# Kernel optimization log

Measured on AMD Instinct MI355X. Metric: run time of the kernel, lower is better.

## Reference

```python
import jax, jax.numpy as jnp
import numpy as np

B, S, D = 4, 2048, 1024


def setup_inputs() -> dict:
    key = jax.random.key(0)
    k1, k2, k3, k4 = jax.random.split(key, 4)
    scale = 1.0 / np.sqrt(D)
    return {
        "X_emb": jax.random.normal(k1, (B, S, D), dtype=jnp.float32),
        "W_q": jax.random.normal(k2, (D, D), dtype=jnp.float32) * scale,
        "W_k": jax.random.normal(k3, (D, D), dtype=jnp.float32) * scale,
        "W_v": jax.random.normal(k4, (D, D), dtype=jnp.float32) * scale,
    }


def reference(X_emb, W_q, W_k, W_v):
    # nn.Linear(bias=False): x @ W.T
    Xq = jnp.einsum('bsd,ed->bse', X_emb, W_q)
    Xk = jnp.einsum('bsd,ed->bse', X_emb, W_k)
    Xv = jnp.einsum('bsd,ed->bse', X_emb, W_v)
    S_len = X_emb.shape[-2]
    # scores [B, S, S]; causal mask (strict upper triangle -> -inf)
    att = jnp.einsum('bqe,bke->bqk', Xq, Xk)
    causal = jnp.tril(jnp.ones((S_len, S_len), dtype=bool))
    att = jnp.where(causal, att, -jnp.inf)
    # note: original masks before scaling; -inf / sqrt(d) is still -inf
    att = att / jnp.sqrt(jnp.asarray(Xk.shape[-1], att.dtype))
    w = jax.nn.softmax(att, axis=-1)
    return jnp.einsum('bqk,bke->bqe', w, Xv)
```

## Files before the change

kernel.cpp:

```cpp
#include <hip/hip_runtime.h>
#include <stdint.h>
#include <math.h>

typedef __attribute__((ext_vector_type(8))) __bf16 bf16x8;
typedef __attribute__((ext_vector_type(4))) float f32x4;

__device__ __forceinline__ unsigned short f2bf(float f) {
    unsigned u = __float_as_uint(f);
    u += 0x7FFF + ((u >> 16) & 1);
    return (unsigned short)(u >> 16);
}

__global__ __launch_bounds__(256)
void f32_to_bf16_k(const float* __restrict__ in, unsigned short* __restrict__ out, int n4) {
    int i = blockIdx.x * blockDim.x + threadIdx.x;
    int stride = gridDim.x * blockDim.x;
    for (; i < n4; i += stride) {
        float4 v = reinterpret_cast<const float4*>(in)[i];
        ushort4 o;
        o.x = f2bf(v.x); o.y = f2bf(v.y); o.z = f2bf(v.z); o.w = f2bf(v.w);
        reinterpret_cast<ushort4*>(out)[i] = o;
    }
}

__global__ __launch_bounds__(256)
void w_convert_k(const float* __restrict__ Wq, const float* __restrict__ Wk,
                 const float* __restrict__ Wv, unsigned short* __restrict__ out, int n4) {
    const float* src = blockIdx.y == 0 ? Wq : (blockIdx.y == 1 ? Wk : Wv);
    unsigned short* dst = out + (size_t)blockIdx.y * n4 * 4;
    int i = blockIdx.x * blockDim.x + threadIdx.x;
    int stride = gridDim.x * blockDim.x;
    for (; i < n4; i += stride) {
        float4 v = reinterpret_cast<const float4*>(src)[i];
        ushort4 o;
        o.x = f2bf(v.x); o.y = f2bf(v.y); o.z = f2bf(v.z); o.w = f2bf(v.w);
        reinterpret_cast<ushort4*>(dst)[i] = o;
    }
}

__device__ __forceinline__ void gload16(const unsigned short* g, unsigned short* l) {
    __builtin_amdgcn_global_load_lds(
        (const __attribute__((address_space(1))) unsigned int*)g,
        (__attribute__((address_space(3))) unsigned int*)l, 16, 0, 0);
}

template <typename CT, int MODE>
__global__ __launch_bounds__(256, 2)
void gemm8(const unsigned short* __restrict__ A, const unsigned short* __restrict__ B,
           CT* __restrict__ C, int lda, int ldb, int ldc, int K,
           long long sA, long long sB, long long sC, float scale, int totj)
{
    constexpr int BM = 128, BN = 128;
    constexpr int FM = 4, FN = 4;

    const int nbx = gridDim.x;
    const int nwg = nbx * gridDim.y;
    const int orig = blockIdx.y * nbx + blockIdx.x;
    const int q8 = nwg >> 3, r8 = nwg & 7;
    const int xcd = orig & 7, idx = orig >> 3;
    const int work = (xcd < r8 ? xcd * (q8 + 1) : r8 * (q8 + 1) + (xcd - r8) * q8) + idx;

    A += (long long)blockIdx.z * sA;
    B += (long long)blockIdx.z * sB;
    C += (long long)blockIdx.z * sC;

    __shared__ unsigned short As[2][BM * 64];
    __shared__ unsigned short Bs[2][BN * 64];

    const int t    = threadIdx.x;
    const int lane = t & 63;
    const int wid  = t >> 6;
    const int wm   = wid >> 1, wn = wid & 1;
    const int rsel = lane & 15;
    const int gsel = lane >> 4;
    const int srow = t >> 3;
    const int swz  = ((t & 7) ^ (srow & 7)) * 8;

    auto run_tile = [&](int br, int bc, int kmax, bool first) {
        const int m0 = br * BM, n0 = bc * BN;
        f32x4 acc[FM][FN];
#pragma unroll
        for (int m = 0; m < FM; ++m)
#pragma unroll
            for (int n = 0; n < FN; ++n) acc[m][n] = (f32x4){0.f, 0.f, 0.f, 0.f};

        const unsigned short* gpA[4];
        const unsigned short* gpB[4];
#pragma unroll
        for (int i = 0; i < 4; ++i) {
            gpA[i] = A + (long long)(m0 + srow + 32 * i) * lda + swz;
            gpB[i] = B + (long long)(n0 + srow + 32 * i) * ldb + swz;
        }

        auto stage = [&](int buf) {
#pragma unroll
            for (int i = 0; i < 4; ++i)
                gload16(gpA[i], &As[buf][i * 2048 + t * 8]);
#pragma unroll
            for (int i = 0; i < 4; ++i)
                gload16(gpB[i], &Bs[buf][i * 2048 + t * 8]);
#pragma unroll
            for (int i = 0; i < 4; ++i) { gpA[i] += 64; gpB[i] += 64; }
        };

        const int nk = kmax >> 6;
        if (!first) {
            __builtin_amdgcn_s_barrier();
            __builtin_amdgcn_sched_barrier(0);
        }
        stage(0);

        for (int kt = 0; kt < nk; ++kt) {
            const int c = kt & 1;
            __builtin_amdgcn_s_barrier();
            __builtin_amdgcn_sched_barrier(0);
            if (kt + 1 < nk) {
                stage(c ^ 1);
                asm volatile("s_waitcnt vmcnt(8)" ::: "memory");
            } else {
                asm volatile("s_waitcnt vmcnt(0)" ::: "memory");
            }
            __builtin_amdgcn_s_barrier();
            __builtin_amdgcn_sched_barrier(0);

            bf16x8 aF[FM][2], bF[FN][2];
#pragma unroll
            for (int m = 0; m < FM; ++m)
#pragma unroll
                for (int ks = 0; ks < 2; ++ks) {
                    int r  = wm * (FM * 16) + m * 16 + rsel;
                    int cc = ks * 4 + gsel;
                    aF[m][ks] = *reinterpret_cast<const bf16x8*>(
                        &As[c][r * 64 + ((cc ^ (r & 7)) * 8)]);
                }
#pragma unroll
            for (int n = 0; n < FN; ++n)
#pragma unroll
                for (int ks = 0; ks < 2; ++ks) {
                    int rb = wn * (FN * 16) + n * 16 + rsel;
                    int cc = ks * 4 + gsel;
                    bF[n][ks] = *reinterpret_cast<const bf16x8*>(
                        &Bs[c][rb * 64 + ((cc ^ (rb & 7)) * 8)]);
                }

            __builtin_amdgcn_s_setprio(1);
#pragma unroll
            for (int m = 0; m < FM; ++m)
#pragma unroll
                for (int n = 0; n < FN; ++n)
#pragma unroll
                    for (int ks = 0; ks < 2; ++ks)
                        acc[m][n] = __builtin_amdgcn_mfma_f32_16x16x32_bf16(
                            aF[m][ks], bF[n][ks], acc[m][n], 0, 0, 0);
            __builtin_amdgcn_s_setprio(0);
        }

        const int rowl = gsel * 4;
#pragma unroll
        for (int m = 0; m < FM; ++m) {
#pragma unroll
            for (int n = 0; n < FN; ++n) {
#pragma unroll
                for (int i = 0; i < 4; ++i) {
                    int r  = m0 + wm * (FM * 16) + m * 16 + rowl + i;
                    int cI = n0 + wn * (FN * 16) + n * 16 + rsel;
                    float v = acc[m][n][i] * scale;
                    if constexpr (sizeof(CT) == 2)
                        ((unsigned short*)C)[(long long)r * ldc + cI] = f2bf(v);
                    else
                        ((float*)C)[(long long)r * ldc + cI] = v;
                }
            }
        }
    };

    auto tri = [&](int w, int& br, int& bc) {
        int rr = (int)((sqrtf(8.0f * (float)w + 1.0f) - 1.0f) * 0.5f);
        while ((rr + 1) * (rr + 2) / 2 <= w) ++rr;
        while (rr * (rr + 1) / 2 > w) --rr;
        br = rr; bc = w - rr * (rr + 1) / 2;
    };

    if constexpr (MODE == 0) {
        run_tile(work / nbx, work % nbx, K, true);
    } else if constexpr (MODE == 1) {
        int br, bc;
        tri(work, br, bc);
        run_tile(br, bc, K, true);
        const int e = work >> 4;
        if ((work & 15) == 8 && nwg + e < totj) {
            tri(nwg + e, br, bc);
            run_tile(br, bc, K, false);
        }
    } else {
        const int s = work & 1, pp = work >> 1;
        const int col = pp & 7, rp = pp >> 3;
        const int row = s ? 15 - rp : rp;
        run_tile(row, col, (row + 1) * BM, true);
    }
}

__device__ __forceinline__ float waveMax(float v) {
#pragma unroll
    for (int o = 32; o > 0; o >>= 1) v = fmaxf(v, __shfl_xor(v, o, 64));
    return v;
}
__device__ __forceinline__ float waveSum(float v) {
#pragma unroll
    for (int o = 32; o > 0; o >>= 1) v += __shfl_xor(v, o, 64);
    return v;
}

__global__ __launch_bounds__(256)
void softmax_causal(const float* __restrict__ S, unsigned short* __restrict__ P, int Slen) {
    __shared__ float e[2048];
    __shared__ float red[4];
    long long row = blockIdx.x;
    int q = (int)(row % Slen);
    const float* srow = S + row * (long long)Slen;
    unsigned short* prow = P + row * (long long)Slen;
    int len = q + 1;
    int t = threadIdx.x;

    int nfull = len >> 2;
    float mx = -3.0e38f;
    for (int i = t; i < nfull; i += 256) {
        float4 v = reinterpret_cast<const float4*>(srow)[i];
        e[4 * i + 0] = v.x; e[4 * i + 1] = v.y;
        e[4 * i + 2] = v.z; e[4 * i + 3] = v.w;
        mx = fmaxf(fmaxf(fmaxf(mx, v.x), v.y), fmaxf(v.z, v.w));
    }
    if (t < (len & 3)) {
        float v = srow[nfull * 4 + t];
        e[nfull * 4 + t] = v;
        mx = fmaxf(mx, v);
    }
    mx = waveMax(mx);
    if ((t & 63) == 0) red[t >> 6] = mx;
    __syncthreads();
    mx = fmaxf(fmaxf(red[0], red[1]), fmaxf(red[2], red[3]));

    float sum = 0.f;
    for (int k = t; k < len; k += 256) {
        float v = __expf(e[k] - mx);
        e[k] = v;
        sum += v;
    }
    sum = waveSum(sum);
    __syncthreads();
    if ((t & 63) == 0) red[t >> 6] = sum;
    __syncthreads();
    sum = red[0] + red[1] + red[2] + red[3];
    float inv = 1.0f / sum;

    int wlim = ((q >> 7) + 1) << 7;
    __syncthreads();
    for (int i = t; i < (wlim >> 2); i += 256) {
        int k = 4 * i;
        ushort4 o;
        o.x = (k + 0 < len) ? f2bf(e[k + 0] * inv) : (unsigned short)0;
        o.y = (k + 1 < len) ? f2bf(e[k + 1] * inv) : (unsigned short)0;
        o.z = (k + 2 < len) ? f2bf(e[k + 2] * inv) : (unsigned short)0;
        o.w = (k + 3 < len) ? f2bf(e[k + 3] * inv) : (unsigned short)0;
        reinterpret_cast<ushort4*>(prow)[i] = o;
    }
}

extern "C" void kernel_launch(void* const* d_in, const int* in_sizes, int n_in,
                              void* d_out, int out_size, void* d_ws, size_t ws_size,
                              hipStream_t stream) {
    const int B = 4, S = 2048, D = 1024;
    const float* X  = (const float*)d_in[0];
    const float* Wq = (const float*)d_in[1];
    const float* Wk = (const float*)d_in[2];
    const float* Wv = (const float*)d_in[3];
    float* out = (float*)d_out;

    char* ws = (char*)d_ws;
    unsigned short* Xb  = (unsigned short*)ws; ws += (size_t)B * S * D * 2;
    unsigned short* Wqb = (unsigned short*)ws; ws += (size_t)D * D * 2;
    unsigned short* Wkb = (unsigned short*)ws; ws += (size_t)D * D * 2;
    unsigned short* Wvb = (unsigned short*)ws; ws += (size_t)D * D * 2;
    unsigned short* Qb  = (unsigned short*)ws; ws += (size_t)B * S * D * 2;
    unsigned short* Kb  = (unsigned short*)ws; ws += (size_t)B * S * D * 2;
    unsigned short* Vt  = (unsigned short*)ws; ws += (size_t)B * S * D * 2;
    float*          Sc  = (float*)ws;          ws += (size_t)B * S * S * 4;
    unsigned short* P   = (unsigned short*)ws; ws += (size_t)B * S * S * 2;

    f32_to_bf16_k<<<2048, 256, 0, stream>>>(X, Xb, B * S * D / 4);
    w_convert_k<<<dim3(512, 3), 256, 0, stream>>>(Wq, Wk, Wv, Wqb, D * D / 4);

    dim3 blk(256);
    gemm8<unsigned short, 0><<<dim3(D / 128, B * S / 128, 2), blk, 0, stream>>>(
        Xb, Wqb, Qb, D, D, D, D, 0, (long long)D * D, (long long)B * S * D, 1.0f, 0);

    gemm8<unsigned short, 0><<<dim3(S / 128, D / 128, B), blk, 0, stream>>>(
        Wvb, Xb, Vt, D, D, S, D, 0, (long long)S * D, (long long)D * S, 1.0f, 0);

    gemm8<float, 1><<<dim3(8, 16, B), blk, 0, stream>>>(
        Qb, Kb, Sc, D, D, S, D, (long long)S * D, (long long)S * D, (long long)S * S,
        0.03125f, 136);

    softmax_causal<<<B * S, 256, 0, stream>>>(Sc, P, S);

    gemm8<float, 3><<<dim3(8, 16, B), blk, 0, stream>>>(
        P, Vt, out, S, S, D, S, (long long)S * S, (long long)D * S, (long long)S * D,
        1.0f, 0);
}
```

Baseline: 176.1 us.

## Deepen GEMM pipeline to four K=32 stages and store scores in bf16

Measured after the change: 203.6 us. +15.6%, slower.

```diff
diff --git a/kernel.cpp b/kernel.cpp
--- a/kernel.cpp
+++ b/kernel.cpp
@@ -9,6 +9,9 @@
     unsigned u = __float_as_uint(f);
     u += 0x7FFF + ((u >> 16) & 1);
     return (unsigned short)(u >> 16);
+}
+__device__ __forceinline__ float bf2f(unsigned short u) {
+    return __uint_as_float((unsigned)u << 16);
 }
 
 __global__ __launch_bounds__(256)
@@ -64,8 +67,8 @@
     B += (long long)blockIdx.z * sB;
     C += (long long)blockIdx.z * sC;
 
-    __shared__ unsigned short As[2][BM * 64];
-    __shared__ unsigned short Bs[2][BN * 64];
+    __shared__ unsigned short As[4][BM * 32];
+    __shared__ unsigned short Bs[4][BN * 32];
 
     const int t    = threadIdx.x;
     const int lane = t & 63;
@@ -73,8 +76,8 @@
     const int wm   = wid >> 1, wn = wid & 1;
     const int rsel = lane & 15;
     const int gsel = lane >> 4;
-    const int srow = t >> 3;
-    const int swz  = ((t & 7) ^ (srow & 7)) * 8;
+    const int srow = t >> 2;
+    const int swz  = ((t & 3) ^ (srow & 3)) * 8;
 
     auto run_tile = [&](int br, int bc, int kmax, bool first) {
         const int m0 = br * BM, n0 = bc * BN;
@@ -84,74 +87,64 @@
 #pragma unroll
             for (int n = 0; n < FN; ++n) acc[m][n] = (f32x4){0.f, 0.f, 0.f, 0.f};
 
-        const unsigned short* gpA[4];
-        const unsigned short* gpB[4];
-#pragma unroll
-        for (int i = 0; i < 4; ++i) {
-            gpA[i] = A + (long long)(m0 + srow + 32 * i) * lda + swz;
-            gpB[i] = B + (long long)(n0 + srow + 32 * i) * ldb + swz;
-        }
-
+        const unsigned short* gpA[2];
+        const unsigned short* gpB[2];
+#pragma unroll
+        for (int i = 0; i < 2; ++i) {
+            gpA[i] = A + (long long)(m0 + srow + 64 * i) * lda + swz;
+            gpB[i] = B + (long long)(n0 + srow + 64 * i) * ldb + swz;
+        }
         auto stage = [&](int buf) {
-#pragma unroll
-            for (int i = 0; i < 4; ++i)
-                gload16(gpA[i], &As[buf][i * 2048 + t * 8]);
-#pragma unroll
-            for (int i = 0; i < 4; ++i)
-                gload16(gpB[i], &Bs[buf][i * 2048 + t * 8]);
-#pragma unroll
-            for (int i = 0; i < 4; ++i) { gpA[i] += 64; gpB[i] += 64; }
+            gload16(gpA[0], &As[buf][t * 8]);
+            gload16(gpA[1], &As[buf][2048 + t * 8]);
+            gload16(gpB[0], &Bs[buf][t * 8]);
+            gload16(gpB[1], &Bs[buf][2048 + t * 8]);
+            gpA[0] += 32; gpA[1] += 32; gpB[0] += 32; gpB[1] += 32;
         };
 
-        const int nk = kmax >> 6;
+        const int nk = kmax >> 5;
         if (!first) {
             __builtin_amdgcn_s_barrier();
             __builtin_amdgcn_sched_barrier(0);
         }
         stage(0);
+        if (1 < nk) stage(1);
+        if (2 < nk) stage(2);
 
         for (int kt = 0; kt < nk; ++kt) {
-            const int c = kt & 1;
+            const int c = kt & 3;
             __builtin_amdgcn_s_barrier();
             __builtin_amdgcn_sched_barrier(0);
-            if (kt + 1 < nk) {
-                stage(c ^ 1);
-                asm volatile("s_waitcnt vmcnt(8)" ::: "memory");
-            } else {
-                asm volatile("s_waitcnt vmcnt(0)" ::: "memory");
-            }
+            if (kt + 3 < nk) stage((kt + 3) & 3);
+            const int rem = nk - 1 - kt;
+            if (rem >= 3)      asm volatile("s_waitcnt vmcnt(12)" ::: "memory");
+            else if (rem == 2) asm volatile("s_waitcnt vmcnt(8)"  ::: "memory");
+            else if (rem == 1) asm volatile("s_waitcnt vmcnt(4)"  ::: "memory");
+            else               asm volatile("s_waitcnt vmcnt(0)"  ::: "memory");
             __builtin_amdgcn_s_barrier();
             __builtin_amdgcn_sched_barrier(0);
 
-            bf16x8 aF[FM][2], bF[FN][2];
+            bf16x8 aF[FM], bF[FN];
+#pragma unroll
+            for (int m = 0; m < FM; ++m) {
+                int r = wm * (FM * 16) + m * 16 + rsel;
+                aF[m] = *reinterpret_cast<const bf16x8*>(
+                    &As[c][r * 32 + ((gsel ^ (r & 3)) * 8)]);
+            }
+#pragma unroll
+            for (int n = 0; n < FN; ++n) {
+                int rb = wn * (FN * 16) + n * 16 + rsel;
+                bF[n] = *reinterpret_cast<const bf16x8*>(
+                    &Bs[c][rb * 32 + ((gsel ^ (rb & 3)) * 8)]);
+            }
+
+            __builtin_amdgcn_s_setprio(1);
 #pragma unroll
             for (int m = 0; m < FM; ++m)
 #pragma unroll
-                for (int ks = 0; ks < 2; ++ks) {
-                    int r  = wm * (FM * 16) + m * 16 + rsel;
-                    int cc = ks * 4 + gsel;
-                    aF[m][ks] = *reinterpret_cast<const bf16x8*>(
-                        &As[c][r * 64 + ((cc ^ (r & 7)) * 8)]);
-                }
-#pragma unroll
-            for (int n = 0; n < FN; ++n)
-#pragma unroll
-                for (int ks = 0; ks < 2; ++ks) {
-                    int rb = wn * (FN * 16) + n * 16 + rsel;
-                    int cc = ks * 4 + gsel;
-                    bF[n][ks] = *reinterpret_cast<const bf16x8*>(
-                        &Bs[c][rb * 64 + ((cc ^ (rb & 7)) * 8)]);
-                }
-
-            __builtin_amdgcn_s_setprio(1);
-#pragma unroll
-            for (int m = 0; m < FM; ++m)
-#pragma unroll
                 for (int n = 0; n < FN; ++n)
-#pragma unroll
-                    for (int ks = 0; ks < 2; ++ks)
-                        acc[m][n] = __builtin_amdgcn_mfma_f32_16x16x32_bf16(
-                            aF[m][ks], bF[n][ks], acc[m][n], 0, 0, 0);
+                    acc[m][n] = __builtin_amdgcn_mfma_f32_16x16x32_bf16(
+                        aF[m], bF[n], acc[m][n], 0, 0, 0);
             __builtin_amdgcn_s_setprio(0);
         }
 
@@ -212,27 +205,33 @@
 }
 
 __global__ __launch_bounds__(256)
-void softmax_causal(const float* __restrict__ S, unsigned short* __restrict__ P, int Slen) {
+void softmax_causal(const unsigned short* __restrict__ S, unsigned short* __restrict__ P,
+                    int Slen) {
     __shared__ float e[2048];
     __shared__ float red[4];
     long long row = blockIdx.x;
     int q = (int)(row % Slen);
-    const float* srow = S + row * (long long)Slen;
+    const unsigned short* srow = S + row * (long long)Slen;
     unsigned short* prow = P + row * (long long)Slen;
     int len = q + 1;
     int t = threadIdx.x;
 
-    int nfull = len >> 2;
+    int n8 = len >> 3;
     float mx = -3.0e38f;
-    for (int i = t; i < nfull; i += 256) {
-        float4 v = reinterpret_cast<const float4*>(srow)[i];
-        e[4 * i + 0] = v.x; e[4 * i + 1] = v.y;
-        e[4 * i + 2] = v.z; e[4 * i + 3] = v.w;
-        mx = fmaxf(fmaxf(fmaxf(mx, v.x), v.y), fmaxf(v.z, v.w));
-    }
-    if (t < (len & 3)) {
-        float v = srow[nfull * 4 + t];
-        e[nfull * 4 + t] = v;
+    for (int i = t; i < n8; i += 256) {
+        uint4 v = reinterpret_cast<const uint4*>(srow)[i];
+        float f0 = __uint_as_float(v.x << 16), f1 = __uint_as_float(v.x & 0xffff0000u);
+        float f2 = __uint_as_float(v.y << 16), f3 = __uint_as_float(v.y & 0xffff0000u);
+        float f4 = __uint_as_float(v.z << 16), f5 = __uint_as_float(v.z & 0xffff0000u);
+        float f6 = __uint_as_float(v.w << 16), f7 = __uint_as_float(v.w & 0xffff0000u);
+        e[8 * i + 0] = f0; e[8 * i + 1] = f1; e[8 * i + 2] = f2; e[8 * i + 3] = f3;
+        e[8 * i + 4] = f4; e[8 * i + 5] = f5; e[8 * i + 6] = f6; e[8 * i + 7] = f7;
+        mx = fmaxf(mx, fmaxf(fmaxf(fmaxf(f0, f1), fmaxf(f2, f3)),
+                             fmaxf(fmaxf(f4, f5), fmaxf(f6, f7))));
+    }
+    if (t < (len & 7)) {
+        float v = bf2f(srow[n8 * 8 + t]);
+        e[n8 * 8 + t] = v;
         mx = fmaxf(mx, v);
     }
     mx = waveMax(mx);
@@ -284,7 +283,7 @@
     unsigned short* Qb  = (unsigned short*)ws; ws += (size_t)B * S * D * 2;
     unsigned short* Kb  = (unsigned short*)ws; ws += (size_t)B * S * D * 2;
     unsigned short* Vt  = (unsigned short*)ws; ws += (size_t)B * S * D * 2;
-    float*          Sc  = (float*)ws;          ws += (size_t)B * S * S * 4;
+    unsigned short* Sc  = (unsigned short*)ws; ws += (size_t)B * S * S * 2;
     unsigned short* P   = (unsigned short*)ws; ws += (size_t)B * S * S * 2;
 
     f32_to_bf16_k<<<2048, 256, 0, stream>>>(X, Xb, B * S * D / 4);
@@ -297,7 +296,7 @@
     gemm8<unsigned short, 0><<<dim3(S / 128, D / 128, B), blk, 0, stream>>>(
         Wvb, Xb, Vt, D, D, S, D, 0, (long long)S * D, (long long)D * S, 1.0f, 0);
 
-    gemm8<float, 1><<<dim3(8, 16, B), blk, 0, stream>>>(
+    gemm8<unsigned short, 1><<<dim3(8, 16, B), blk, 0, stream>>>(
         Qb, Kb, Sc, D, D, S, D, (long long)S * D, (long long)S * D, (long long)S * S,
         0.03125f, 136);
 
```

## Store attention scores in bf16, merge conversion kernels, reorder PV tile mapping

Applied to the files above, without the earlier changes.

Result: no change. 173.0 us (-1.8%).

```diff
diff --git a/kernel.cpp b/kernel.cpp
--- a/kernel.cpp
+++ b/kernel.cpp
@@ -10,24 +10,24 @@
     u += 0x7FFF + ((u >> 16) & 1);
     return (unsigned short)(u >> 16);
 }
+__device__ __forceinline__ float bf2f(unsigned short u) {
+    return __uint_as_float((unsigned)u << 16);
+}
 
 __global__ __launch_bounds__(256)
-void f32_to_bf16_k(const float* __restrict__ in, unsigned short* __restrict__ out, int n4) {
-    int i = blockIdx.x * blockDim.x + threadIdx.x;
-    int stride = gridDim.x * blockDim.x;
-    for (; i < n4; i += stride) {
-        float4 v = reinterpret_cast<const float4*>(in)[i];
-        ushort4 o;
-        o.x = f2bf(v.x); o.y = f2bf(v.y); o.z = f2bf(v.z); o.w = f2bf(v.w);
-        reinterpret_cast<ushort4*>(out)[i] = o;
-    }
-}
-
-__global__ __launch_bounds__(256)
-void w_convert_k(const float* __restrict__ Wq, const float* __restrict__ Wk,
-                 const float* __restrict__ Wv, unsigned short* __restrict__ out, int n4) {
-    const float* src = blockIdx.y == 0 ? Wq : (blockIdx.y == 1 ? Wk : Wv);
-    unsigned short* dst = out + (size_t)blockIdx.y * n4 * 4;
+void convert_all_k(const float* __restrict__ X, const float* __restrict__ Wq,
+                   const float* __restrict__ Wk, const float* __restrict__ Wv,
+                   unsigned short* __restrict__ Xb, unsigned short* __restrict__ Wb,
+                   int n4x, int n4w) {
+    const float* src;
+    unsigned short* dst;
+    int n4;
+    if (blockIdx.y == 0) { src = X; dst = Xb; n4 = n4x; }
+    else {
+        src = blockIdx.y == 1 ? Wq : (blockIdx.y == 2 ? Wk : Wv);
+        dst = Wb + (size_t)(blockIdx.y - 1) * n4w * 4;
+        n4 = n4w;
+    }
     int i = blockIdx.x * blockDim.x + threadIdx.x;
     int stride = gridDim.x * blockDim.x;
     for (; i < n4; i += stride) {
@@ -193,9 +193,10 @@
             run_tile(br, bc, K, false);
         }
     } else {
-        const int s = work & 1, pp = work >> 1;
-        const int col = pp & 7, rp = pp >> 3;
-        const int row = s ? 15 - rp : rp;
+        const int chunk = work >> 4;
+        const int lo    = work & 15;
+        const int col   = work & 7;
+        const int row   = (lo < 8) ? chunk : 15 - chunk;
         run_tile(row, col, (row + 1) * BM, true);
     }
 }
@@ -212,27 +213,33 @@
 }
 
 __global__ __launch_bounds__(256)
-void softmax_causal(const float* __restrict__ S, unsigned short* __restrict__ P, int Slen) {
+void softmax_causal(const unsigned short* __restrict__ S, unsigned short* __restrict__ P,
+                    int Slen) {
     __shared__ float e[2048];
     __shared__ float red[4];
     long long row = blockIdx.x;
     int q = (int)(row % Slen);
-    const float* srow = S + row * (long long)Slen;
+    const unsigned short* srow = S + row * (long long)Slen;
     unsigned short* prow = P + row * (long long)Slen;
     int len = q + 1;
     int t = threadIdx.x;
 
-    int nfull = len >> 2;
+    int n8 = len >> 3;
     float mx = -3.0e38f;
-    for (int i = t; i < nfull; i += 256) {
-        float4 v = reinterpret_cast<const float4*>(srow)[i];
-        e[4 * i + 0] = v.x; e[4 * i + 1] = v.y;
-        e[4 * i + 2] = v.z; e[4 * i + 3] = v.w;
-        mx = fmaxf(fmaxf(fmaxf(mx, v.x), v.y), fmaxf(v.z, v.w));
-    }
-    if (t < (len & 3)) {
-        float v = srow[nfull * 4 + t];
-        e[nfull * 4 + t] = v;
+    for (int i = t; i < n8; i += 256) {
+        uint4 v = reinterpret_cast<const uint4*>(srow)[i];
+        float f0 = __uint_as_float(v.x << 16), f1 = __uint_as_float(v.x & 0xffff0000u);
+        float f2 = __uint_as_float(v.y << 16), f3 = __uint_as_float(v.y & 0xffff0000u);
+        float f4 = __uint_as_float(v.z << 16), f5 = __uint_as_float(v.z & 0xffff0000u);
+        float f6 = __uint_as_float(v.w << 16), f7 = __uint_as_float(v.w & 0xffff0000u);
+        e[8 * i + 0] = f0; e[8 * i + 1] = f1; e[8 * i + 2] = f2; e[8 * i + 3] = f3;
+        e[8 * i + 4] = f4; e[8 * i + 5] = f5; e[8 * i + 6] = f6; e[8 * i + 7] = f7;
+        mx = fmaxf(mx, fmaxf(fmaxf(fmaxf(f0, f1), fmaxf(f2, f3)),
+                             fmaxf(fmaxf(f4, f5), fmaxf(f6, f7))));
+    }
+    if (t < (len & 7)) {
+        float v = bf2f(srow[n8 * 8 + t]);
+        e[n8 * 8 + t] = v;
         mx = fmaxf(mx, v);
     }
     mx = waveMax(mx);
@@ -284,11 +291,11 @@
     unsigned short* Qb  = (unsigned short*)ws; ws += (size_t)B * S * D * 2;
     unsigned short* Kb  = (unsigned short*)ws; ws += (size_t)B * S * D * 2;
     unsigned short* Vt  = (unsigned short*)ws; ws += (size_t)B * S * D * 2;
-    float*          Sc  = (float*)ws;          ws += (size_t)B * S * S * 4;
+    unsigned short* Sc  = (unsigned short*)ws; ws += (size_t)B * S * S * 2;
     unsigned short* P   = (unsigned short*)ws; ws += (size_t)B * S * S * 2;
 
-    f32_to_bf16_k<<<2048, 256, 0, stream>>>(X, Xb, B * S * D / 4);
-    w_convert_k<<<dim3(512, 3), 256, 0, stream>>>(Wq, Wk, Wv, Wqb, D * D / 4);
+    convert_all_k<<<dim3(2048, 4), 256, 0, stream>>>(
+        X, Wq, Wk, Wv, Xb, Wqb, B * S * D / 4, D * D / 4);
 
     dim3 blk(256);
     gemm8<unsigned short, 0><<<dim3(D / 128, B * S / 128, 2), blk, 0, stream>>>(
@@ -297,7 +304,7 @@
     gemm8<unsigned short, 0><<<dim3(S / 128, D / 128, B), blk, 0, stream>>>(
         Wvb, Xb, Vt, D, D, S, D, 0, (long long)S * D, (long long)D * S, 1.0f, 0);
 
-    gemm8<float, 1><<<dim3(8, 16, B), blk, 0, stream>>>(
+    gemm8<unsigned short, 1><<<dim3(8, 16, B), blk, 0, stream>>>(
         Qb, Kb, Sc, D, D, S, D, (long long)S * D, (long long)S * D, (long long)S * S,
         0.03125f, 136);
 
```
